# Optimization experiments

Hardware: AMD Instinct MI355X
Metric: run time of the kernel (lower is better)

## Reference

```python
import jax, jax.numpy as jnp
import numpy as np


def setup_inputs() -> dict:
    key = jax.random.key(0)
    B, N = 4, 32768
    xyz = jax.random.normal(key, (B, N, 3), dtype=jnp.float32)
    return {"xyz": xyz, "K": 16, "nqueries": 2048}


def reference(xyz, K, nqueries):
    # xyz: (b, n, 3). Deterministic strided pick of nqueries query points
    # (stand-in for the KD-tree's distance-pick sampling), then brute-force KNN.
    b, n, _ = xyz.shape
    stride = n // nqueries
    q_idx = jnp.arange(nqueries) * stride          # (nq,)
    pts = xyz[:, q_idx, :]                          # (b, nq, 3) sampled query points
    # pairwise squared distances (b, nq, n)
    d = jnp.sum((pts[:, :, None, :] - xyz[:, None, :, :]) ** 2, axis=-1)
    _, idx = jax.lax.top_k(-d, K)                   # (b, nq, K) nearest-neighbor indices
    idx = idx.astype(jnp.int64)[..., None]          # (b, nq, K, 1) matches expand_dims(..., 3)
    return idx, pts
```

## Files before the change

kernel.cpp:

```cpp
#include <hip/hip_runtime.h>
#include <stdint.h>

#define NPTS  32768
#define NQ    2048
#define KNN   16
#define NB    4
#define BLOCK 256
#define WPB   4
#define PPL   8
#define ITERS (NPTS / (64 * PPL))

__device__ __forceinline__ int dpp_shr1_i(int x) {
    return __builtin_amdgcn_update_dpp(x, x, 0x111, 0xf, 0xf, false);
}
__device__ __forceinline__ float dpp_shr1_f(float x) {
    return __int_as_float(dpp_shr1_i(__float_as_int(x)));
}
__device__ __forceinline__ float readlane_f(float x, int l) {
    return __int_as_float(__builtin_amdgcn_readlane(__float_as_int(x), l));
}

template <int T>
__device__ __forceinline__ void insert_all(float d, int p, int lane,
                                           float& ld, int& li, float& tau, float& tg)
{
    unsigned long long rem = __ballot(d <= tau);
    while (rem) {
        const int srcl = __ffsll(rem) - 1;
        const float wd = readlane_f(d, srcl);
        const int   wi = __builtin_amdgcn_readlane(p, srcl);
        const bool less = (ld < wd) || (ld == wd && li < wi);
        const unsigned long long lm = __ballot(less);
        const int pos = __popc((unsigned)((lm >> (16 * T)) & 0xffffull));
        const float pld = dpp_shr1_f(ld);
        const int   pli = dpp_shr1_i(li);
        if ((lane >> 4) == T) {
            const int gl = lane & 15;
            if (gl == pos)      { ld = wd;  li = wi;  }
            else if (gl > pos)  { ld = pld; li = pli; }
        }
        tau = readlane_f(ld, 16 * T + 15);
        tg  = tau * 1.00001f;
        rem &= rem - 1;
        if (rem) rem &= __ballot(d <= tau);
    }
}

__device__ __forceinline__ void load6(float4 dst[6], const float4* p) {
    #pragma unroll
    for (int t = 0; t < 6; ++t) dst[t] = p[t];
}

__device__ __forceinline__ void step(const float4 c[6], int pb, int lane,
                                     float qx0, float qy0, float qz0,
                                     float qx1, float qy1, float qz1,
                                     float& ld, int& li,
                                     float& tau0, float& tau1,
                                     float& tg0, float& tg1)
{
    float px[PPL], py[PPL], pz[PPL];
    px[0] = c[0].x; py[0] = c[0].y; pz[0] = c[0].z;
    px[1] = c[0].w; py[1] = c[1].x; pz[1] = c[1].y;
    px[2] = c[1].z; py[2] = c[1].w; pz[2] = c[2].x;
    px[3] = c[2].y; py[3] = c[2].z; pz[3] = c[2].w;
    px[4] = c[3].x; py[4] = c[3].y; pz[4] = c[3].z;
    px[5] = c[3].w; py[5] = c[4].x; pz[5] = c[4].y;
    px[6] = c[4].z; py[6] = c[4].w; pz[6] = c[5].x;
    px[7] = c[5].y; py[7] = c[5].z; pz[7] = c[5].w;

    unsigned long long m0[PPL], m1[PPL], any = 0;
    #pragma unroll
    for (int j = 0; j < PPL; ++j) {
        const float ax = px[j] - qx0, ay = py[j] - qy0, az = pz[j] - qz0;
        const float g0 = __fmaf_rn(az, az, __fmaf_rn(ay, ay, __fmul_rn(ax, ax)));
        m0[j] = __ballot(g0 <= tg0);
        const float bx = px[j] - qx1, by = py[j] - qy1, bz = pz[j] - qz1;
        const float g1 = __fmaf_rn(bz, bz, __fmaf_rn(by, by, __fmul_rn(bx, bx)));
        m1[j] = __ballot(g1 <= tg1);
        any |= m0[j] | m1[j];
    }
    if (any) {
        #pragma unroll
        for (int j = 0; j < PPL; ++j) {
            if (m0[j]) {
                const float dx = __fadd_rn(px[j], -qx0);
                const float dy = __fadd_rn(py[j], -qy0);
                const float dz = __fadd_rn(pz[j], -qz0);
                const float d  = __fadd_rn(
                    __fadd_rn(__fmul_rn(dx, dx), __fmul_rn(dy, dy)),
                    __fmul_rn(dz, dz));
                insert_all<0>(d, pb + j, lane, ld, li, tau0, tg0);
            }
        }
        #pragma unroll
        for (int j = 0; j < PPL; ++j) {
            if (m1[j]) {
                const float dx = __fadd_rn(px[j], -qx1);
                const float dy = __fadd_rn(py[j], -qy1);
                const float dz = __fadd_rn(pz[j], -qz1);
                const float d  = __fadd_rn(
                    __fadd_rn(__fmul_rn(dx, dx), __fmul_rn(dy, dy)),
                    __fmul_rn(dz, dz));
                insert_all<1>(d, pb + j, lane, ld, li, tau1, tg1);
            }
        }
    }
}

__global__ __launch_bounds__(BLOCK, 4) void knn_kernel(const float* __restrict__ xyz,
                                                       float* __restrict__ out_idx,
                                                       float* __restrict__ out_pts)
{
    const int tid  = threadIdx.x;
    const int lane = tid & 63;
    const int wv   = tid >> 6;
    const int w    = blockIdx.x * WPB + wv;
    const int b    = w >> 10;
    const int pr   = w & 1023;
    const size_t base = (size_t)b * NPTS * 3;

    const int qp0 = pr << 5;
    const float qx0 = xyz[base + 3 * qp0 + 0];
    const float qy0 = xyz[base + 3 * qp0 + 1];
    const float qz0 = xyz[base + 3 * qp0 + 2];
    const float qx1 = xyz[base + 3 * qp0 + 48];
    const float qy1 = xyz[base + 3 * qp0 + 49];
    const float qz1 = xyz[base + 3 * qp0 + 50];

    const int g0 = b * NQ + (pr << 1);
    if (lane == 0) {
        out_pts[3 * g0 + 0] = qx0;
        out_pts[3 * g0 + 1] = qy0;
        out_pts[3 * g0 + 2] = qz0;
        out_pts[3 * g0 + 3] = qx1;
        out_pts[3 * g0 + 4] = qy1;
        out_pts[3 * g0 + 5] = qz1;
    }

    float ld = __builtin_inff();  int li = 0x7fffffff;
    float tau0 = __builtin_inff(), tau1 = __builtin_inff();
    float tg0  = __builtin_inff(), tg1  = __builtin_inff();

    const float4* lp = (const float4*)(xyz + base) + 6 * lane;

    float4 A[6], Bf[6];
    load6(A, lp);
    for (int k = 0; k < ITERS; k += 2) {
        load6(Bf, lp + 384);
        step(A, (k << 9) + PPL * lane, lane,
             qx0, qy0, qz0, qx1, qy1, qz1, ld, li, tau0, tau1, tg0, tg1);
        if (k + 2 < ITERS)
            load6(A, lp + 768);
        step(Bf, ((k + 1) << 9) + PPL * lane, lane,
             qx0, qy0, qz0, qx1, qy1, qz1, ld, li, tau0, tau1, tg0, tg1);
        lp += 768;
    }

    if (lane < 2 * KNN) {
        out_idx[(size_t)g0 * KNN + lane] = (float)li;
    }
}

extern "C" void kernel_launch(void* const* d_in, const int* in_sizes, int n_in,
                              void* d_out, int out_size, void* d_ws, size_t ws_size,
                              hipStream_t stream) {
    const float* xyz = (const float*)d_in[0];
    float* out = (float*)d_out;
    float* out_idx = out;
    float* out_pts = out + (size_t)NB * NQ * KNN;

    const int blocks = (NB * NQ / 2) / WPB;
    knn_kernel<<<blocks, BLOCK, 0, stream>>>(xyz, out_idx, out_pts);
}
```

Baseline: 195.7 us.

## Split each query pair's scan across two waves and merge top-K in LDS

Each query pair is now handled by two waves, and each wave scans half of the point cloud. The two partial top-16 lists are merged through shared memory with a rank-by-count step. This doubles the wave count and halves the serial scan length per wave, which should improve latency hiding. In exchange, each half starts with a looser threshold, so more insertions may happen, and a block barrier plus merge is added. The launch-bounds occupancy hint goes from 4 to 8, and the threshold-guard update is moved out of the insert loop.

```diff
diff --git a/kernel.cpp b/kernel.cpp
--- a/kernel.cpp
+++ b/kernel.cpp
@@ -6,9 +6,9 @@
 #define KNN   16
 #define NB    4
 #define BLOCK 256
-#define WPB   4
+#define HALF  16384
 #define PPL   8
-#define ITERS (NPTS / (64 * PPL))
+#define ITERS (HALF / (64 * PPL))
 
 __device__ __forceinline__ int dpp_shr1_i(int x) {
     return __builtin_amdgcn_update_dpp(x, x, 0x111, 0xf, 0xf, false);
@@ -40,10 +40,10 @@
             else if (gl > pos)  { ld = pld; li = pli; }
         }
         tau = readlane_f(ld, 16 * T + 15);
-        tg  = tau * 1.00001f;
         rem &= rem - 1;
         if (rem) rem &= __ballot(d <= tau);
     }
+    tg = tau * 1.00001f;
 }
 
 __device__ __forceinline__ void load6(float4 dst[6], const float4* p) {
@@ -107,16 +107,21 @@
     }
 }
 
-__global__ __launch_bounds__(BLOCK, 4) void knn_kernel(const float* __restrict__ xyz,
+__global__ __launch_bounds__(BLOCK, 8) void knn_kernel(const float* __restrict__ xyz,
                                                        float* __restrict__ out_idx,
                                                        float* __restrict__ out_pts)
 {
-    const int tid  = threadIdx.x;
-    const int lane = tid & 63;
-    const int wv   = tid >> 6;
-    const int w    = blockIdx.x * WPB + wv;
-    const int b    = w >> 10;
-    const int pr   = w & 1023;
+    __shared__ float d_buf[2][2][2][KNN];
+    __shared__ int   i_buf[2][2][2][KNN];
+
+    const int tid   = threadIdx.x;
+    const int lane  = tid & 63;
+    const int wv    = tid >> 6;
+    const int pairw = wv >> 1;
+    const int h     = wv & 1;
+    const int qpg   = blockIdx.x * 2 + pairw;
+    const int b     = qpg >> 10;
+    const int pr    = qpg & 1023;
     const size_t base = (size_t)b * NPTS * 3;
 
     const int qp0 = pr << 5;
@@ -128,7 +133,7 @@
     const float qz1 = xyz[base + 3 * qp0 + 50];
 
     const int g0 = b * NQ + (pr << 1);
-    if (lane == 0) {
+    if (h == 0 && lane == 0) {
         out_pts[3 * g0 + 0] = qx0;
         out_pts[3 * g0 + 1] = qy0;
         out_pts[3 * g0 + 2] = qz0;
@@ -141,23 +146,43 @@
     float tau0 = __builtin_inff(), tau1 = __builtin_inff();
     float tg0  = __builtin_inff(), tg1  = __builtin_inff();
 
-    const float4* lp = (const float4*)(xyz + base) + 6 * lane;
+    const float4* lp = (const float4*)(xyz + base) + h * (HALF * 3 / 4) + 6 * lane;
+    const int pbase = h * HALF + PPL * lane;
 
     float4 A[6], Bf[6];
     load6(A, lp);
     for (int k = 0; k < ITERS; k += 2) {
         load6(Bf, lp + 384);
-        step(A, (k << 9) + PPL * lane, lane,
+        step(A, pbase + (k << 9), lane,
              qx0, qy0, qz0, qx1, qy1, qz1, ld, li, tau0, tau1, tg0, tg1);
         if (k + 2 < ITERS)
             load6(A, lp + 768);
-        step(Bf, ((k + 1) << 9) + PPL * lane, lane,
+        step(Bf, pbase + ((k + 1) << 9), lane,
              qx0, qy0, qz0, qx1, qy1, qz1, ld, li, tau0, tau1, tg0, tg1);
         lp += 768;
     }
 
-    if (lane < 2 * KNN) {
-        out_idx[(size_t)g0 * KNN + lane] = (float)li;
+    if (lane < 32) {
+        const int t = lane >> 4;
+        d_buf[pairw][t][h][lane & 15] = ld;
+        i_buf[pairw][t][h][lane & 15] = li;
+    }
+    __syncthreads();
+
+    if (h == 0) {
+        const int t = lane >> 5;
+        const int s = lane & 31;
+        const float d = d_buf[pairw][t][s >> 4][s & 15];
+        const int   i = i_buf[pairw][t][s >> 4][s & 15];
+        int cnt = 0;
+        #pragma unroll
+        for (int r = 0; r < 32; ++r) {
+            const float od = d_buf[pairw][t][r >> 4][r & 15];
+            const int   oi = i_buf[pairw][t][r >> 4][r & 15];
+            cnt += ((od < d) || (od == d && oi < i)) ? 1 : 0;
+        }
+        if (cnt < KNN)
+            out_idx[(size_t)(g0 + t) * KNN + cnt] = (float)i;
     }
 }
 
@@ -169,6 +194,6 @@
     float* out_idx = out;
     float* out_pts = out + (size_t)NB * NQ * KNN;
 
-    const int blocks = (NB * NQ / 2) / WPB;
+    const int blocks = (NB * NQ / 2) / 2;
     knn_kernel<<<blocks, BLOCK, 0, stream>>>(xyz, out_idx, out_pts);
 }
```

Measured after the change: 705.4 us. +260.4%, slower.
